# Kernel tuning notes

Measured on AMD Instinct MI355X. Metric: run time of the kernel, lower is better.

The kernel has to match this reference:

```python
import jax, jax.numpy as jnp
import numpy as np

N = 50000    # nodes
P = 4        # meta-paths
E = 800000   # edges per meta-path (avg degree 16)
IN = 256     # in_size
OUT = 128    # out_size


def _xavier(key, shape, gain=1.0):
    fan_in, fan_out = shape[-2], shape[-1]
    lim = gain * np.sqrt(6.0 / (fan_in + fan_out))
    return jax.random.uniform(key, shape, jnp.float32, -lim, lim)


def setup_inputs() -> dict:
    key = jax.random.key(0)
    ks = jax.random.split(key, 8)
    x = jax.random.normal(ks[0], (N, IN), jnp.float32)
    src = jax.random.randint(ks[1], (P, E), 0, N)
    dst = jax.random.randint(ks[2], (P, E), 0, N)
    # per-meta-path GraphConv weight/bias (dgl default: xavier weight, zero bias)
    W = _xavier(ks[3], (P, IN, OUT))
    b_conv = jnp.zeros((P, OUT), jnp.float32)
    # semantic attention vectors, xavier with gain=1.414 on shape (1, OUT)
    att_lim = 1.414 * np.sqrt(6.0 / (1 + OUT))
    att = jax.random.uniform(ks[4], (P, OUT), jnp.float32, -att_lim, att_lim)
    fc_w = _xavier(ks[5], (OUT, OUT))
    fc_b = jnp.zeros((OUT,), jnp.float32)
    h_bias = jnp.zeros((OUT,), jnp.float32)
    return {"x": x, "W": W, "b_conv": b_conv, "att": att,
            "fc_w": fc_w, "fc_b": fc_b, "h_bias": h_bias,
            "src": src, "dst": dst}


def _graphconv(x, src, dst, W, b):
    # dgl GraphConv, norm='both', allow_zero_in_degree=True (degrees clamped to 1)
    ones_e = jnp.ones(src.shape[0], x.dtype)
    deg_out = jnp.maximum(jax.ops.segment_sum(ones_e, src, num_segments=N), 1.0)
    deg_in = jnp.maximum(jax.ops.segment_sum(ones_e, dst, num_segments=N), 1.0)
    # weight applied before aggregation (in_size > out_size path) -- same math
    xw = (x * jax.lax.rsqrt(deg_out)[:, None]) @ W          # [N, OUT]
    agg = jax.ops.segment_sum(xw[src], dst, num_segments=N)  # [N, OUT]
    return agg * jax.lax.rsqrt(deg_in)[:, None] + b


def reference(x, W, b_conv, att, fc_w, fc_b, h_bias, src, dst):
    # one GraphConv per meta-path (P is a small fixed structural set)
    hs = [_graphconv(x, src[i], dst[i], W[i], b_conv[i]) for i in range(P)]
    # semantic attention: sp_i = tanh(fc(h_i)).mean(0); beta_i = att_i . sp_i
    sp = jnp.stack([jnp.tanh(h @ fc_w.T + fc_b).mean(axis=0) for h in hs])  # [P, OUT]
    beta = jax.nn.softmax(jnp.sum(att * sp, axis=-1))  # [P]
    h = hs[0] * beta[0]
    for i in range(1, P):
        h = h + hs[i] * beta[i]
    # epilogue: bias (self_loop=False, activation=None, dropout eval = identity)
    return h + h_bias
```

## Files before the change

### kernel.cpp

```cpp
#include <hip/hip_runtime.h>
#include <math.h>

#define N_NODES 50000
#define P_PATHS 4
#define E_EDGES 800000
#define IN_F 256
#define OUT_F 128
#define NPB 128
#define NBUCK 391
#define NCHUNK 200
#define CHUNK_E (E_EDGES / NCHUNK)
#define GBLK 391
#define DSL 20
#define QTR 4
#define Q_N 12500
#define Q_W 6250
#define BKP 72
#define FP 136
#define RSB 196

typedef unsigned short ushort_t;
typedef unsigned int uint_t;
typedef float f32x4 __attribute__((ext_vector_type(4)));
typedef short s16x8 __attribute__((ext_vector_type(8)));

__device__ __forceinline__ ushort_t f2bf(float f) {
    uint_t u = __float_as_uint(f);
    return (ushort_t)((u + 0x7FFFu + ((u >> 16) & 1u)) >> 16);
}
__device__ __forceinline__ float bf2f(ushort_t h) {
    return __uint_as_float(((uint_t)h) << 16);
}
__device__ __forceinline__ uint4 pack8(const float4 f0, const float4 f1) {
    uint4 w;
    w.x = (uint_t)f2bf(f0.x) | ((uint_t)f2bf(f0.y) << 16);
    w.y = (uint_t)f2bf(f0.z) | ((uint_t)f2bf(f0.w) << 16);
    w.z = (uint_t)f2bf(f1.x) | ((uint_t)f2bf(f1.y) << 16);
    w.w = (uint_t)f2bf(f1.z) | ((uint_t)f2bf(f1.w) << 16);
    return w;
}
__device__ __forceinline__ float fast_tanh(float v) {
    v = fminf(fmaxf(v, -20.f), 20.f);
    float ex = __expf(2.f * v);
    return (ex - 1.f) / (ex + 1.f);
}
__device__ __forceinline__ void acc4(float4& a, uint2 w) {
    a.x += bf2f((ushort_t)w.x);
    a.y += bf2f((ushort_t)(w.x >> 16));
    a.z += bf2f((ushort_t)w.y);
    a.w += bf2f((ushort_t)(w.y >> 16));
}

__global__ void prep_kernel(const float* __restrict__ W, const float* __restrict__ fcw,
                            ushort_t* __restrict__ Wt, ushort_t* __restrict__ fcwb)
{
    int idx = blockIdx.x * blockDim.x + threadIdx.x;
    if (idx < P_PATHS * IN_F * OUT_F) {
        int p = idx >> 15;
        int r = idx & 32767;
        int k = r >> 7;
        int n = r & 127;
        Wt[((size_t)p << 15) + (size_t)n * IN_F + k] = f2bf(W[idx]);
    }
    if (idx < OUT_F * OUT_F) fcwb[idx] = f2bf(fcw[idx]);
}

__global__ __launch_bounds__(256) void deghist_kernel(const int* __restrict__ src,
                                                      const int* __restrict__ dst,
                                                      uint_t* __restrict__ dhist,
                                                      uint_t* __restrict__ bcounts)
{
    __shared__ uint_t cnt[Q_W];
    int sl = blockIdx.x, q = blockIdx.y, p = blockIdx.z;
    int t = threadIdx.x;
    if (q == QTR) {
        for (int i = t; i < NBUCK; i += 256) cnt[i] = 0;
        __syncthreads();
        const int4* d4 = (const int4*)(dst + (size_t)p * E_EDGES + (size_t)sl * (E_EDGES / DSL));
        for (int i = t; i < E_EDGES / DSL / 4; i += 256) {
            int4 v = d4[i];
            atomicAdd(&cnt[v.x >> 7], 1u);
            atomicAdd(&cnt[v.y >> 7], 1u);
            atomicAdd(&cnt[v.z >> 7], 1u);
            atomicAdd(&cnt[v.w >> 7], 1u);
        }
        __syncthreads();
        for (int i = t; i < NBUCK; i += 256)
            if (cnt[i]) atomicAdd(&bcounts[p * NBUCK + i], cnt[i]);
        return;
    }
    int nbase = q * Q_N;
    for (int i = t; i < Q_W; i += 256) cnt[i] = 0;
    __syncthreads();
    const int4* s4 = (const int4*)(src + (size_t)p * E_EDGES + (size_t)sl * (E_EDGES / DSL));
    for (int i = t; i < E_EDGES / DSL / 4; i += 256) {
        int4 v = s4[i];
        uint_t r;
        r = (uint_t)(v.x - nbase); if (r < Q_N) atomicAdd(&cnt[r >> 1], 1u << ((r & 1) * 16));
        r = (uint_t)(v.y - nbase); if (r < Q_N) atomicAdd(&cnt[r >> 1], 1u << ((r & 1) * 16));
        r = (uint_t)(v.z - nbase); if (r < Q_N) atomicAdd(&cnt[r >> 1], 1u << ((r & 1) * 16));
        r = (uint_t)(v.w - nbase); if (r < Q_N) atomicAdd(&cnt[r >> 1], 1u << ((r & 1) * 16));
    }
    __syncthreads();
    uint_t* outp = dhist + (((size_t)p * QTR + q) * DSL + sl) * Q_W;
    for (int i = t; i < Q_W; i += 256) outp[i] = cnt[i];
}

__global__ __launch_bounds__(1024) void rsout_bscan_kernel(const uint_t* __restrict__ dhist,
                                                           float* __restrict__ rsout,
                                                           const uint_t* __restrict__ bcounts,
                                                           int* __restrict__ bstart,
                                                           int* __restrict__ bcursor)
{
    int t = threadIdx.x;
    if (blockIdx.x == RSB) {
        __shared__ int a[2048], b[2048];
        for (int i = t; i < 2048; i += 1024)
            a[i] = (i < P_PATHS * NBUCK) ? (int)bcounts[i] : 0;
        __syncthreads();
        int* pin = a; int* pout = b;
        for (int off = 1; off < 2048; off <<= 1) {
            for (int i = t; i < 2048; i += 1024)
                pout[i] = pin[i] + (i >= off ? pin[i - off] : 0);
            __syncthreads();
            int* tmp = pin; pin = pout; pout = tmp;
        }
        for (int i = t; i < P_PATHS * NBUCK; i += 1024) {
            int st = pin[i] - (int)bcounts[i];
            bstart[i] = st;
            bcursor[i] = st;
        }
        if (t == 0) bstart[P_PATHS * NBUCK] = pin[P_PATHS * NBUCK - 1];
        return;
    }
    int idx = blockIdx.x * 1024 + t;
    if (idx >= P_PATHS * QTR * Q_W) return;
    int ph = idx / Q_W;
    int w  = idx % Q_W;
    const uint_t* base = dhist + (size_t)ph * DSL * Q_W + w;
    uint_t s = 0;
#pragma unroll
    for (int sl = 0; sl < DSL; ++sl) s += base[(size_t)sl * Q_W];
    int p = ph >> 2, q = ph & 3;
    int node = q * Q_N + 2 * w;
    uint_t c0 = s & 0xFFFFu, c1 = s >> 16;
    rsout[(size_t)p * N_NODES + node]     = rsqrtf((float)(c0 ? c0 : 1u));
    rsout[(size_t)p * N_NODES + node + 1] = rsqrtf((float)(c1 ? c1 : 1u));
}

__global__ __launch_bounds__(256) void bscatter_kernel(const int* __restrict__ src,
                                                       const int* __restrict__ dst,
                                                       int* __restrict__ bcursor,
                                                       uint_t* __restrict__ ebuf)
{
    __shared__ uint_t bh[NBUCK];
    __shared__ uint_t lbase[NBUCK];
    int p = blockIdx.y;
    int t = threadIdx.x;
    int sub = p * E_EDGES;
    int* bcursor_p = bcursor + p * NBUCK;
    uint_t* ebuf_p = ebuf + (size_t)p * E_EDGES;
    for (int i = t; i < NBUCK; i += 256) bh[i] = 0;
    __syncthreads();
    size_t ebase = (size_t)p * E_EDGES + (size_t)blockIdx.x * CHUNK_E;
    const int4* d4 = (const int4*)(dst + ebase);
    const int4* s4 = (const int4*)(src + ebase);
    for (int i = t; i < CHUNK_E / 4; i += 256) {
        int4 v = d4[i];
        atomicAdd(&bh[v.x >> 7], 1u);
        atomicAdd(&bh[v.y >> 7], 1u);
        atomicAdd(&bh[v.z >> 7], 1u);
        atomicAdd(&bh[v.w >> 7], 1u);
    }
    __syncthreads();
    for (int i = t; i < NBUCK; i += 256) {
        uint_t c = bh[i];
        lbase[i] = c ? (uint_t)(atomicAdd(&bcursor_p[i], (int)c) - sub) : 0u;
        bh[i] = 0;
    }
    __syncthreads();
    for (int i = t; i < CHUNK_E / 4; i += 256) {
        int4 d = d4[i];
        int4 s = s4[i];
        { int bk = d.x >> 7; uint_t pos = lbase[bk] + atomicAdd(&bh[bk], 1u); ebuf_p[pos] = (uint_t)s.x | ((uint_t)(d.x & 127) << 16); }
        { int bk = d.y >> 7; uint_t pos = lbase[bk] + atomicAdd(&bh[bk], 1u); ebuf_p[pos] = (uint_t)s.y | ((uint_t)(d.y & 127) << 16); }
        { int bk = d.z >> 7; uint_t pos = lbase[bk] + atomicAdd(&bh[bk], 1u); ebuf_p[pos] = (uint_t)s.z | ((uint_t)(d.z & 127) << 16); }
        { int bk = d.w >> 7; uint_t pos = lbase[bk] + atomicAdd(&bh[bk], 1u); ebuf_p[pos] = (uint_t)s.w | ((uint_t)(d.w & 127) << 16); }
    }
}

__global__ __launch_bounds__(256) void blocal_kernel(const uint_t* __restrict__ ebuf,
                                                     const int* __restrict__ bstart,
                                                     ushort_t* __restrict__ eidx2,
                                                     int* __restrict__ rsn)
{
    __shared__ uint_t hist[NPB];
    __shared__ uint_t cur[NPB];
    __shared__ uint_t sa[NPB], sb[NPB];
    int bkt = blockIdx.x;
    int p = blockIdx.y;
    int t = threadIdx.x;
    int sub = p * E_EDGES;
    const uint_t* ebuf_p = ebuf + (size_t)p * E_EDGES;
    ushort_t* eidx2_p = eidx2 + (size_t)p * E_EDGES;
    int* rsn_p = rsn + (size_t)p * (N_NODES + 1);
    if (t < NPB) hist[t] = 0;
    __syncthreads();
    int r0 = bstart[p * NBUCK + bkt] - sub;
    int r1 = bstart[p * NBUCK + bkt + 1] - sub;
    for (int e = r0 + t; e < r1; e += 256)
        atomicAdd(&hist[ebuf_p[e] >> 16], 1u);
    __syncthreads();
    if (t < NPB) sa[t] = hist[t];
    __syncthreads();
    uint_t* pin = sa; uint_t* pout = sb;
    for (int off = 1; off < NPB; off <<= 1) {
        if (t < NPB) pout[t] = pin[t] + (t >= off ? pin[t - off] : 0u);
        __syncthreads();
        uint_t* tmp = pin; pin = pout; pout = tmp;
    }
    if (t < NPB) {
        uint_t ex = pin[t] - hist[t];
        int node = bkt * NPB + t;
        if (node < N_NODES) rsn_p[node] = r0 + (int)ex;
        cur[t] = ex;
    }
    if (bkt == NBUCK - 1 && t == 0) rsn_p[N_NODES] = r1;
    __syncthreads();
    for (int e = r0 + t; e < r1; e += 256) {
        uint_t pk = ebuf_p[e];
        int dl = (int)(pk >> 16);
        uint_t pos = atomicAdd(&cur[dl], 1u);
        eidx2_p[r0 + pos] = (ushort_t)(pk & 0xFFFFu);
    }
}

__global__ __launch_bounds__(256) void gemm_xall_kernel(const float* __restrict__ x,
                                                        const ushort_t* __restrict__ Wt,
                                                        const float* __restrict__ rsout,
                                                        ushort_t* __restrict__ xwb)
{
    __shared__ ushort_t As[128 * BKP];
    __shared__ ushort_t Bs[128 * BKP];
    int m0 = blockIdx.x * 128;
    int t = threadIdx.x;
    int wid = t >> 6, lane = t & 63;
    int wr = wid >> 1, wc = wid & 1;
    int srow = t >> 1, h32 = (t & 1) * 32;
    int gr = m0 + srow;
    for (int pp = 0; pp < 2; ++pp) {
        int p = blockIdx.y * 2 + pp;
        const ushort_t* Wp = Wt + ((size_t)p << 15);
        f32x4 acc[4][4] = {};
        for (int kt = 0; kt < 4; ++kt) {
            __syncthreads();
            {
                const float* ap = x + (size_t)gr * IN_F + kt * 64 + h32;
#pragma unroll
                for (int c = 0; c < 4; ++c) {
                    float4 f0 = make_float4(0.f, 0.f, 0.f, 0.f), f1 = f0;
                    if (gr < N_NODES) {
                        f0 = *(const float4*)(ap + c * 8);
                        f1 = *(const float4*)(ap + c * 8 + 4);
                    }
                    *(uint4*)&As[srow * BKP + h32 + c * 8] = pack8(f0, f1);
                }
            }
            {
                const ushort_t* bp = Wp + (size_t)srow * IN_F + kt * 64 + h32;
#pragma unroll
                for (int c = 0; c < 4; ++c)
                    *(uint4*)&Bs[srow * BKP + h32 + c * 8] = *(const uint4*)(bp + c * 8);
            }
            __syncthreads();
#pragma unroll
            for (int k0 = 0; k0 < 64; k0 += 32) {
                s16x8 aF[4], bF[4];
                int kk = k0 + (lane >> 4) * 8;
#pragma unroll
                for (int m = 0; m < 4; ++m)
                    aF[m] = *(const s16x8*)&As[(wr * 64 + m * 16 + (lane & 15)) * BKP + kk];
#pragma unroll
                for (int n = 0; n < 4; ++n)
                    bF[n] = *(const s16x8*)&Bs[(wc * 64 + n * 16 + (lane & 15)) * BKP + kk];
#pragma unroll
                for (int m = 0; m < 4; ++m)
#pragma unroll
                    for (int n = 0; n < 4; ++n)
                        acc[m][n] = __builtin_amdgcn_mfma_f32_16x16x32_bf16(aF[m], bF[n], acc[m][n], 0, 0, 0);
            }
        }
        ushort_t* xp = xwb + (size_t)p * N_NODES * OUT_F;
        const float* rp = rsout + (size_t)p * N_NODES;
#pragma unroll
        for (int m = 0; m < 4; ++m) {
#pragma unroll
            for (int i = 0; i < 4; ++i) {
                int row = m0 + wr * 64 + m * 16 + (lane >> 4) * 4 + i;
                if (row < N_NODES) {
                    float rs = rp[row];
#pragma unroll
                    for (int n = 0; n < 4; ++n) {
                        int col = wc * 64 + n * 16 + (lane & 15);
                        xp[(size_t)row * OUT_F + col] = f2bf(acc[m][n][i] * rs);
                    }
                }
            }
        }
    }
}

__global__ __launch_bounds__(256) void gather_kernel(const ushort_t* __restrict__ xwb,
                                                     const ushort_t* __restrict__ eidx2,
                                                     const int* __restrict__ rsn,
                                                     const float* __restrict__ bconv,
                                                     uint2* __restrict__ hb)
{
    int hw = threadIdx.x >> 5;
    int lane = threadIdx.x & 31;
    int p = blockIdx.y;
    int n0 = (blockIdx.x * 8 + hw) * 2;
    const int* rsn_p = rsn + (size_t)p * (N_NODES + 1);
    const ushort_t* eidx2_p = eidx2 + (size_t)p * E_EDGES;
    int bA = rsn_p[n0], mid = rsn_p[n0 + 1], eB = rsn_p[n0 + 2];
    const uint2* base = (const uint2*)xwb + (size_t)p * N_NODES * 32 + lane;
    float4 aA = make_float4(0.f, 0.f, 0.f, 0.f);
    float4 aB = make_float4(0.f, 0.f, 0.f, 0.f);
    int iA = bA, iB = mid;
    while (iA + 4 <= mid && iB + 4 <= eB) {
        int sA0 = eidx2_p[iA], sA1 = eidx2_p[iA + 1], sA2 = eidx2_p[iA + 2], sA3 = eidx2_p[iA + 3];
        int sB0 = eidx2_p[iB], sB1 = eidx2_p[iB + 1], sB2 = eidx2_p[iB + 2], sB3 = eidx2_p[iB + 3];
        uint2 wA0 = base[(size_t)sA0 * 32];
        uint2 wA1 = base[(size_t)sA1 * 32];
        uint2 wA2 = base[(size_t)sA2 * 32];
        uint2 wA3 = base[(size_t)sA3 * 32];
        uint2 wB0 = base[(size_t)sB0 * 32];
        uint2 wB1 = base[(size_t)sB1 * 32];
        uint2 wB2 = base[(size_t)sB2 * 32];
        uint2 wB3 = base[(size_t)sB3 * 32];
        acc4(aA, wA0); acc4(aA, wA1); acc4(aA, wA2); acc4(aA, wA3);
        acc4(aB, wB0); acc4(aB, wB1); acc4(aB, wB2); acc4(aB, wB3);
        iA += 4; iB += 4;
    }
    for (; iA + 4 <= mid; iA += 4) {
        int s0 = eidx2_p[iA], s1 = eidx2_p[iA + 1], s2 = eidx2_p[iA + 2], s3 = eidx2_p[iA + 3];
        uint2 w0 = base[(size_t)s0 * 32];
        uint2 w1 = base[(size_t)s1 * 32];
        uint2 w2 = base[(size_t)s2 * 32];
        uint2 w3 = base[(size_t)s3 * 32];
        acc4(aA, w0); acc4(aA, w1); acc4(aA, w2); acc4(aA, w3);
    }
    for (; iA < mid; ++iA) {
        uint2 w = base[(size_t)eidx2_p[iA] * 32];
        acc4(aA, w);
    }
    for (; iB + 4 <= eB; iB += 4) {
        int s0 = eidx2_p[iB], s1 = eidx2_p[iB + 1], s2 = eidx2_p[iB + 2], s3 = eidx2_p[iB + 3];
        uint2 w0 = base[(size_t)s0 * 32];
        uint2 w1 = base[(size_t)s1 * 32];
        uint2 w2 = base[(size_t)s2 * 32];
        uint2 w3 = base[(size_t)s3 * 32];
        acc4(aB, w0); acc4(aB, w1); acc4(aB, w2); acc4(aB, w3);
    }
    for (; iB < eB; ++iB) {
        uint2 w = base[(size_t)eidx2_p[iB] * 32];
        acc4(aB, w);
    }
    int dA = mid - bA, dB = eB - mid;
    float scA = rsqrtf((float)(dA > 0 ? dA : 1));
    float scB = rsqrtf((float)(dB > 0 ? dB : 1));
    float4 bc = *(const float4*)(bconv + (size_t)p * OUT_F + lane * 4);
    uint2 oA, oB;
    oA.x = (uint_t)f2bf(fmaf(aA.x, scA, bc.x)) | ((uint_t)f2bf(fmaf(aA.y, scA, bc.y)) << 16);
    oA.y = (uint_t)f2bf(fmaf(aA.z, scA, bc.z)) | ((uint_t)f2bf(fmaf(aA.w, scA, bc.w)) << 16);
    oB.x = (uint_t)f2bf(fmaf(aB.x, scB, bc.x)) | ((uint_t)f2bf(fmaf(aB.y, scB, bc.y)) << 16);
    oB.y = (uint_t)f2bf(fmaf(aB.z, scB, bc.z)) | ((uint_t)f2bf(fmaf(aB.w, scB, bc.w)) << 16);
    hb[((size_t)p * N_NODES + n0) * 32 + lane]     = oA;
    hb[((size_t)p * N_NODES + n0 + 1) * 32 + lane] = oB;
}

__global__ __launch_bounds__(256) void fc_mfma_kernel(const ushort_t* __restrict__ hb,
                                                      const ushort_t* __restrict__ fcwb,
                                                      const float* __restrict__ fcb,
                                                      float* __restrict__ partial)
{
    __shared__ ushort_t As[128 * FP];
    __shared__ ushort_t Bs[128 * FP];
    __shared__ float red[2][128];
    int m0 = blockIdx.x * 128;
    int t = threadIdx.x;
    int wid = t >> 6, lane = t & 63;
    int wr = wid >> 1, wc = wid & 1;
    int srow = t >> 1, half = (t & 1) * 16;
    int gr = m0 + srow;
    {
#pragma unroll
        for (int c = 0; c < 4; ++c) {
            int kb = c * 32 + half;
            const ushort_t* bp = fcwb + (size_t)srow * OUT_F + kb;
            *(uint4*)&Bs[srow * FP + kb]     = *(const uint4*)(bp);
            *(uint4*)&Bs[srow * FP + kb + 8] = *(const uint4*)(bp + 8);
        }
    }
    for (int p = 0; p < P_PATHS; ++p) {
        __syncthreads();
        const ushort_t* hp = hb + (size_t)p * N_NODES * OUT_F;
#pragma unroll
        for (int c = 0; c < 4; ++c) {
            int kb = c * 32 + half;
            uint4 w0 = make_uint4(0, 0, 0, 0), w1 = w0;
            if (gr < N_NODES) {
                const ushort_t* ap = hp + (size_t)gr * OUT_F + kb;
                w0 = *(const uint4*)(ap);
                w1 = *(const uint4*)(ap + 8);
            }
            *(uint4*)&As[srow * FP + kb]     = w0;
            *(uint4*)&As[srow * FP + kb + 8] = w1;
        }
        __syncthreads();
        f32x4 acc[4][4] = {};
#pragma unroll
        for (int k0 = 0; k0 < OUT_F; k0 += 32) {
            s16x8 aF[4], bF[4];
            int kk = k0 + (lane >> 4) * 8;
#pragma unroll
            for (int m = 0; m < 4; ++m)
                aF[m] = *(const s16x8*)&As[(wr * 64 + m * 16 + (lane & 15)) * FP + kk];
#pragma unroll
            for (int n = 0; n < 4; ++n)
                bF[n] = *(const s16x8*)&Bs[(wc * 64 + n * 16 + (lane & 15)) * FP + kk];
#pragma unroll
            for (int m = 0; m < 4; ++m)
#pragma unroll
                for (int n = 0; n < 4; ++n)
                    acc[m][n] = __builtin_amdgcn_mfma_f32_16x16x32_bf16(aF[m], bF[n], acc[m][n], 0, 0, 0);
        }
#pragma unroll
        for (int n = 0; n < 4; ++n) {
            int col = wc * 64 + n * 16 + (lane & 15);
            float fb = fcb[col];
            float s = 0.f;
#pragma unroll
            for (int m = 0; m < 4; ++m)
#pragma unroll
                for (int i = 0; i < 4; ++i) {
                    int row = m0 + wr * 64 + m * 16 + (lane >> 4) * 4 + i;
                    if (row < N_NODES) s += fast_tanh(acc[m][n][i] + fb);
                }
            s += __shfl_xor(s, 16);
            s += __shfl_xor(s, 32);
            if (lane < 16) red[wr][col] = s;
        }
        __syncthreads();
        if (t < 128)
            partial[((size_t)p * GBLK + blockIdx.x) * OUT_F + t] = red[0][t] + red[1][t];
    }
}

__global__ __launch_bounds__(512) void beta_reduce_kernel(const float* __restrict__ partial,
                                                          const float* __restrict__ att,
                                                          float* __restrict__ beta)
{
    int t = threadIdx.x;
    int p = t >> 7, c = t & 127;
    float s = 0.f;
    for (int i = 0; i < GBLK; ++i)
        s += partial[((size_t)p * GBLK + i) * OUT_F + c];
    float v = att[p * OUT_F + c] * (s * (1.0f / N_NODES));
    __shared__ float red[512];
    red[t] = v;
    __syncthreads();
    for (int off = 64; off >= 1; off >>= 1) {
        if (c < off) red[t] += red[t + off];
        __syncthreads();
    }
    if (t == 0) {
        float w[P_PATHS], mx = -1e30f;
        for (int q = 0; q < P_PATHS; ++q) { w[q] = red[q * 128]; mx = fmaxf(mx, w[q]); }
        float sum = 0.f;
        for (int q = 0; q < P_PATHS; ++q) { w[q] = expf(w[q] - mx); sum += w[q]; }
        for (int q = 0; q < P_PATHS; ++q) beta[q] = w[q] / sum;
    }
}

__global__ void combine_kernel(const uint_t* __restrict__ hb, const float* __restrict__ hbias,
                               const float* __restrict__ beta, float* __restrict__ out)
{
    int idx = blockIdx.x * blockDim.x + threadIdx.x;
    if (idx >= N_NODES * 64) return;
    int n = idx >> 6;
    int w = idx & 63;
    float2 hbv = *(const float2*)(hbias + 2 * w);
    float r0 = hbv.x, r1 = hbv.y;
#pragma unroll
    for (int p = 0; p < P_PATHS; ++p) {
        float bp = beta[p];
        uint_t v = hb[((size_t)p * N_NODES + n) * 64 + w];
        r0 = fmaf(bp, bf2f((ushort_t)v), r0);
        r1 = fmaf(bp, bf2f((ushort_t)(v >> 16)), r1);
    }
    *(float2*)(out + (size_t)n * OUT_F + 2 * w) = make_float2(r0, r1);
}

extern "C" void kernel_launch(void* const* d_in, const int* in_sizes, int n_in,
                              void* d_out, int out_size, void* d_ws, size_t ws_size,
                              hipStream_t stream)
{
    const float* x      = (const float*)d_in[0];
    const float* W      = (const float*)d_in[1];
    const float* b_conv = (const float*)d_in[2];
    const float* att    = (const float*)d_in[3];
    const float* fc_w   = (const float*)d_in[4];
    const float* fc_b   = (const float*)d_in[5];
    const float* h_bias = (const float*)d_in[6];
    const int*   src    = (const int*)d_in[7];
    const int*   dst    = (const int*)d_in[8];
    float* out = (float*)d_out;
    float* ws  = (float*)d_ws;

    size_t off_rsout   = 0;
    size_t off_partial = off_rsout + (size_t)P_PATHS * N_NODES;
    size_t off_beta    = off_partial + (size_t)P_PATHS * GBLK * OUT_F;
    size_t off_i32     = (off_beta + 4 + 63) & ~(size_t)63;
    size_t i_bstart  = 0;
    size_t i_bcursor = 1600;
    size_t i_bcounts = 3200;
    size_t i_rsn     = 4800;
    size_t i_dhist   = 204864;
    size_t i_ebuf    = i_dhist + (size_t)P_PATHS * QTR * DSL * Q_W;
    size_t n_ints    = i_ebuf + (size_t)P_PATHS * E_EDGES;
    size_t off_u16   = off_i32 + ((n_ints + 63) & ~(size_t)63);
    size_t u_hb    = 0;
    size_t u_xwb   = u_hb + (size_t)P_PATHS * N_NODES * OUT_F;
    size_t u_eidx2 = u_xwb + (size_t)P_PATHS * N_NODES * OUT_F;
    size_t u_Wt    = u_eidx2 + (size_t)P_PATHS * E_EDGES;
    size_t u_fcwb  = u_Wt + (size_t)P_PATHS * IN_F * OUT_F;

    float* rsout   = ws + off_rsout;
    float* partial = ws + off_partial;
    float* beta    = ws + off_beta;
    int*   ibase   = (int*)(ws + off_i32);
    int*    bstart  = ibase + i_bstart;
    int*    bcursor = ibase + i_bcursor;
    uint_t* bcounts = (uint_t*)(ibase + i_bcounts);
    int*    rsn     = ibase + i_rsn;
    uint_t* dhist   = (uint_t*)(ibase + i_dhist);
    uint_t* ebuf    = (uint_t*)(ibase + i_ebuf);
    ushort_t* ubase = (ushort_t*)(ws + off_u16);
    ushort_t* hb    = ubase + u_hb;
    ushort_t* xwb   = ubase + u_xwb;
    ushort_t* eidx2 = ubase + u_eidx2;
    ushort_t* Wt    = ubase + u_Wt;
    ushort_t* fcwb  = ubase + u_fcwb;

    hipMemsetAsync(bcounts, 0, (size_t)P_PATHS * NBUCK * sizeof(uint_t), stream);

    prep_kernel<<<(P_PATHS * IN_F * OUT_F + 255) / 256, 256, 0, stream>>>(W, fc_w, Wt, fcwb);
    deghist_kernel<<<dim3(DSL, QTR + 1, P_PATHS), 256, 0, stream>>>(src, dst, dhist, bcounts);
    rsout_bscan_kernel<<<RSB + 1, 1024, 0, stream>>>(dhist, rsout, bcounts, bstart, bcursor);

    gemm_xall_kernel<<<dim3(GBLK, 2), 256, 0, stream>>>(x, Wt, rsout, xwb);
    bscatter_kernel<<<dim3(NCHUNK, P_PATHS), 256, 0, stream>>>(src, dst, bcursor, ebuf);
    blocal_kernel<<<dim3(NBUCK, P_PATHS), 256, 0, stream>>>(ebuf, bstart, eidx2, rsn);
    gather_kernel<<<dim3(N_NODES / 16, P_PATHS), 256, 0, stream>>>(
        xwb, eidx2, rsn, b_conv, (uint2*)hb);
    fc_mfma_kernel<<<GBLK, 256, 0, stream>>>(hb, fcwb, fc_b, partial);

    beta_reduce_kernel<<<1, 512, 0, stream>>>(partial, att, beta);
    combine_kernel<<<(N_NODES * 64 + 255) / 256, 256, 0, stream>>>(
        (const uint_t*)hb, h_bias, beta, out);
}
```

Measured before the change: 316.6 us.

## Fuse prep into deghist, merge gemm with bscatter, widen gather loads

```diff
diff --git a/kernel.cpp b/kernel.cpp
--- a/kernel.cpp
+++ b/kernel.cpp
@@ -44,35 +44,38 @@
     float ex = __expf(2.f * v);
     return (ex - 1.f) / (ex + 1.f);
 }
-__device__ __forceinline__ void acc4(float4& a, uint2 w) {
-    a.x += bf2f((ushort_t)w.x);
-    a.y += bf2f((ushort_t)(w.x >> 16));
-    a.z += bf2f((ushort_t)w.y);
-    a.w += bf2f((ushort_t)(w.y >> 16));
-}
-
-__global__ void prep_kernel(const float* __restrict__ W, const float* __restrict__ fcw,
-                            ushort_t* __restrict__ Wt, ushort_t* __restrict__ fcwb)
-{
-    int idx = blockIdx.x * blockDim.x + threadIdx.x;
-    if (idx < P_PATHS * IN_F * OUT_F) {
-        int p = idx >> 15;
-        int r = idx & 32767;
-        int k = r >> 7;
-        int n = r & 127;
-        Wt[((size_t)p << 15) + (size_t)n * IN_F + k] = f2bf(W[idx]);
-    }
-    if (idx < OUT_F * OUT_F) fcwb[idx] = f2bf(fcw[idx]);
+__device__ __forceinline__ void acc8(float4& a0, float4& a1, uint4 w) {
+    a0.x += bf2f((ushort_t)w.x);  a0.y += bf2f((ushort_t)(w.x >> 16));
+    a0.z += bf2f((ushort_t)w.y);  a0.w += bf2f((ushort_t)(w.y >> 16));
+    a1.x += bf2f((ushort_t)w.z);  a1.y += bf2f((ushort_t)(w.z >> 16));
+    a1.z += bf2f((ushort_t)w.w);  a1.w += bf2f((ushort_t)(w.w >> 16));
 }
 
 __global__ __launch_bounds__(256) void deghist_kernel(const int* __restrict__ src,
                                                       const int* __restrict__ dst,
                                                       uint_t* __restrict__ dhist,
-                                                      uint_t* __restrict__ bcounts)
+                                                      uint_t* __restrict__ bcounts,
+                                                      const float* __restrict__ W,
+                                                      const float* __restrict__ fcw,
+                                                      ushort_t* __restrict__ Wt,
+                                                      ushort_t* __restrict__ fcwb)
 {
     __shared__ uint_t cnt[Q_W];
     int sl = blockIdx.x, q = blockIdx.y, p = blockIdx.z;
     int t = threadIdx.x;
+    if (q == QTR + 1) {
+        int g = (p * DSL + sl) * 256 + t;
+        for (int idx = g; idx < P_PATHS * IN_F * OUT_F; idx += DSL * P_PATHS * 256) {
+            int pp = idx >> 15;
+            int r = idx & 32767;
+            int k = r >> 7;
+            int n = r & 127;
+            Wt[((size_t)pp << 15) + (size_t)n * IN_F + k] = f2bf(W[idx]);
+        }
+        for (int idx = g; idx < OUT_F * OUT_F; idx += DSL * P_PATHS * 256)
+            fcwb[idx] = f2bf(fcw[idx]);
+        return;
+    }
     if (q == QTR) {
         for (int i = t; i < NBUCK; i += 256) cnt[i] = 0;
         __syncthreads();
@@ -148,21 +151,100 @@
     rsout[(size_t)p * N_NODES + node + 1] = rsqrtf((float)(c1 ? c1 : 1u));
 }
 
-__global__ __launch_bounds__(256) void bscatter_kernel(const int* __restrict__ src,
-                                                       const int* __restrict__ dst,
-                                                       int* __restrict__ bcursor,
-                                                       uint_t* __restrict__ ebuf)
-{
-    __shared__ uint_t bh[NBUCK];
-    __shared__ uint_t lbase[NBUCK];
-    int p = blockIdx.y;
+__global__ __launch_bounds__(256) void mid_kernel(const float* __restrict__ x,
+                                                  const ushort_t* __restrict__ Wt,
+                                                  const float* __restrict__ rsout,
+                                                  ushort_t* __restrict__ xwb,
+                                                  const int* __restrict__ src,
+                                                  const int* __restrict__ dst,
+                                                  int* __restrict__ bcursor,
+                                                  uint_t* __restrict__ ebuf)
+{
+    __shared__ ushort_t smem[2 * 128 * BKP];
+    int bx = blockIdx.x;
     int t = threadIdx.x;
+    if (bx < 2 * GBLK) {
+        ushort_t* As = smem;
+        ushort_t* Bs = smem + 128 * BKP;
+        int m0 = (bx % GBLK) * 128;
+        int pair = bx / GBLK;
+        int wid = t >> 6, lane = t & 63;
+        int wr = wid >> 1, wc = wid & 1;
+        int srow = t >> 1, h32 = (t & 1) * 32;
+        int gr = m0 + srow;
+        for (int pp = 0; pp < 2; ++pp) {
+            int p = pair * 2 + pp;
+            const ushort_t* Wp = Wt + ((size_t)p << 15);
+            f32x4 acc[4][4] = {};
+            for (int kt = 0; kt < 4; ++kt) {
+                __syncthreads();
+                {
+                    const float* ap = x + (size_t)gr * IN_F + kt * 64 + h32;
+#pragma unroll
+                    for (int c = 0; c < 4; ++c) {
+                        float4 f0 = make_float4(0.f, 0.f, 0.f, 0.f), f1 = f0;
+                        if (gr < N_NODES) {
+                            f0 = *(const float4*)(ap + c * 8);
+                            f1 = *(const float4*)(ap + c * 8 + 4);
+                        }
+                        *(uint4*)&As[srow * BKP + h32 + c * 8] = pack8(f0, f1);
+                    }
+                }
+                {
+                    const ushort_t* bp = Wp + (size_t)srow * IN_F + kt * 64 + h32;
+#pragma unroll
+                    for (int c = 0; c < 4; ++c)
+                        *(uint4*)&Bs[srow * BKP + h32 + c * 8] = *(const uint4*)(bp + c * 8);
+                }
+                __syncthreads();
+#pragma unroll
+                for (int k0 = 0; k0 < 64; k0 += 32) {
+                    s16x8 aF[4], bF[4];
+                    int kk = k0 + (lane >> 4) * 8;
+#pragma unroll
+                    for (int m = 0; m < 4; ++m)
+                        aF[m] = *(const s16x8*)&As[(wr * 64 + m * 16 + (lane & 15)) * BKP + kk];
+#pragma unroll
+                    for (int n = 0; n < 4; ++n)
+                        bF[n] = *(const s16x8*)&Bs[(wc * 64 + n * 16 + (lane & 15)) * BKP + kk];
+#pragma unroll
+                    for (int m = 0; m < 4; ++m)
+#pragma unroll
+                        for (int n = 0; n < 4; ++n)
+                            acc[m][n] = __builtin_amdgcn_mfma_f32_16x16x32_bf16(aF[m], bF[n], acc[m][n], 0, 0, 0);
+                }
+            }
+            ushort_t* xp = xwb + (size_t)p * N_NODES * OUT_F;
+            const float* rp = rsout + (size_t)p * N_NODES;
+#pragma unroll
+            for (int m = 0; m < 4; ++m) {
+#pragma unroll
+                for (int i = 0; i < 4; ++i) {
+                    int row = m0 + wr * 64 + m * 16 + (lane >> 4) * 4 + i;
+                    if (row < N_NODES) {
+                        float rs = rp[row];
+#pragma unroll
+                        for (int n = 0; n < 4; ++n) {
+                            int col = wc * 64 + n * 16 + (lane & 15);
+                            xp[(size_t)row * OUT_F + col] = f2bf(acc[m][n][i] * rs);
+                        }
+                    }
+                }
+            }
+        }
+        return;
+    }
+    int idx = bx - 2 * GBLK;
+    int p = idx / NCHUNK;
+    int ck = idx % NCHUNK;
+    uint_t* bh    = (uint_t*)smem;
+    uint_t* lbase = bh + NBUCK;
     int sub = p * E_EDGES;
     int* bcursor_p = bcursor + p * NBUCK;
     uint_t* ebuf_p = ebuf + (size_t)p * E_EDGES;
     for (int i = t; i < NBUCK; i += 256) bh[i] = 0;
     __syncthreads();
-    size_t ebase = (size_t)p * E_EDGES + (size_t)blockIdx.x * CHUNK_E;
+    size_t ebase = (size_t)p * E_EDGES + (size_t)ck * CHUNK_E;
     const int4* d4 = (const int4*)(dst + ebase);
     const int4* s4 = (const int4*)(src + ebase);
     for (int i = t; i < CHUNK_E / 4; i += 256) {
@@ -235,148 +317,62 @@
     }
 }
 
-__global__ __launch_bounds__(256) void gemm_xall_kernel(const float* __restrict__ x,
-                                                        const ushort_t* __restrict__ Wt,
-                                                        const float* __restrict__ rsout,
-                                                        ushort_t* __restrict__ xwb)
-{
-    __shared__ ushort_t As[128 * BKP];
-    __shared__ ushort_t Bs[128 * BKP];
-    int m0 = blockIdx.x * 128;
-    int t = threadIdx.x;
-    int wid = t >> 6, lane = t & 63;
-    int wr = wid >> 1, wc = wid & 1;
-    int srow = t >> 1, h32 = (t & 1) * 32;
-    int gr = m0 + srow;
-    for (int pp = 0; pp < 2; ++pp) {
-        int p = blockIdx.y * 2 + pp;
-        const ushort_t* Wp = Wt + ((size_t)p << 15);
-        f32x4 acc[4][4] = {};
-        for (int kt = 0; kt < 4; ++kt) {
-            __syncthreads();
-            {
-                const float* ap = x + (size_t)gr * IN_F + kt * 64 + h32;
-#pragma unroll
-                for (int c = 0; c < 4; ++c) {
-                    float4 f0 = make_float4(0.f, 0.f, 0.f, 0.f), f1 = f0;
-                    if (gr < N_NODES) {
-                        f0 = *(const float4*)(ap + c * 8);
-                        f1 = *(const float4*)(ap + c * 8 + 4);
-                    }
-                    *(uint4*)&As[srow * BKP + h32 + c * 8] = pack8(f0, f1);
-                }
-            }
-            {
-                const ushort_t* bp = Wp + (size_t)srow * IN_F + kt * 64 + h32;
-#pragma unroll
-                for (int c = 0; c < 4; ++c)
-                    *(uint4*)&Bs[srow * BKP + h32 + c * 8] = *(const uint4*)(bp + c * 8);
-            }
-            __syncthreads();
-#pragma unroll
-            for (int k0 = 0; k0 < 64; k0 += 32) {
-                s16x8 aF[4], bF[4];
-                int kk = k0 + (lane >> 4) * 8;
-#pragma unroll
-                for (int m = 0; m < 4; ++m)
-                    aF[m] = *(const s16x8*)&As[(wr * 64 + m * 16 + (lane & 15)) * BKP + kk];
-#pragma unroll
-                for (int n = 0; n < 4; ++n)
-                    bF[n] = *(const s16x8*)&Bs[(wc * 64 + n * 16 + (lane & 15)) * BKP + kk];
-#pragma unroll
-                for (int m = 0; m < 4; ++m)
-#pragma unroll
-                    for (int n = 0; n < 4; ++n)
-                        acc[m][n] = __builtin_amdgcn_mfma_f32_16x16x32_bf16(aF[m], bF[n], acc[m][n], 0, 0, 0);
-            }
-        }
-        ushort_t* xp = xwb + (size_t)p * N_NODES * OUT_F;
-        const float* rp = rsout + (size_t)p * N_NODES;
-#pragma unroll
-        for (int m = 0; m < 4; ++m) {
-#pragma unroll
-            for (int i = 0; i < 4; ++i) {
-                int row = m0 + wr * 64 + m * 16 + (lane >> 4) * 4 + i;
-                if (row < N_NODES) {
-                    float rs = rp[row];
-#pragma unroll
-                    for (int n = 0; n < 4; ++n) {
-                        int col = wc * 64 + n * 16 + (lane & 15);
-                        xp[(size_t)row * OUT_F + col] = f2bf(acc[m][n][i] * rs);
-                    }
-                }
-            }
-        }
-    }
-}
-
 __global__ __launch_bounds__(256) void gather_kernel(const ushort_t* __restrict__ xwb,
                                                      const ushort_t* __restrict__ eidx2,
                                                      const int* __restrict__ rsn,
                                                      const float* __restrict__ bconv,
-                                                     uint2* __restrict__ hb)
+                                                     uint4* __restrict__ hb)
 {
     int hw = threadIdx.x >> 5;
     int lane = threadIdx.x & 31;
+    int sub = lane >> 4;
+    int c16 = lane & 15;
     int p = blockIdx.y;
-    int n0 = (blockIdx.x * 8 + hw) * 2;
+    int n = blockIdx.x * 8 + hw;
     const int* rsn_p = rsn + (size_t)p * (N_NODES + 1);
-    const ushort_t* eidx2_p = eidx2 + (size_t)p * E_EDGES;
-    int bA = rsn_p[n0], mid = rsn_p[n0 + 1], eB = rsn_p[n0 + 2];
-    const uint2* base = (const uint2*)xwb + (size_t)p * N_NODES * 32 + lane;
-    float4 aA = make_float4(0.f, 0.f, 0.f, 0.f);
-    float4 aB = make_float4(0.f, 0.f, 0.f, 0.f);
-    int iA = bA, iB = mid;
-    while (iA + 4 <= mid && iB + 4 <= eB) {
-        int sA0 = eidx2_p[iA], sA1 = eidx2_p[iA + 1], sA2 = eidx2_p[iA + 2], sA3 = eidx2_p[iA + 3];
-        int sB0 = eidx2_p[iB], sB1 = eidx2_p[iB + 1], sB2 = eidx2_p[iB + 2], sB3 = eidx2_p[iB + 3];
-        uint2 wA0 = base[(size_t)sA0 * 32];
-        uint2 wA1 = base[(size_t)sA1 * 32];
-        uint2 wA2 = base[(size_t)sA2 * 32];
-        uint2 wA3 = base[(size_t)sA3 * 32];
-        uint2 wB0 = base[(size_t)sB0 * 32];
-        uint2 wB1 = base[(size_t)sB1 * 32];
-        uint2 wB2 = base[(size_t)sB2 * 32];
-        uint2 wB3 = base[(size_t)sB3 * 32];
-        acc4(aA, wA0); acc4(aA, wA1); acc4(aA, wA2); acc4(aA, wA3);
-        acc4(aB, wB0); acc4(aB, wB1); acc4(aB, wB2); acc4(aB, wB3);
-        iA += 4; iB += 4;
-    }
-    for (; iA + 4 <= mid; iA += 4) {
-        int s0 = eidx2_p[iA], s1 = eidx2_p[iA + 1], s2 = eidx2_p[iA + 2], s3 = eidx2_p[iA + 3];
-        uint2 w0 = base[(size_t)s0 * 32];
-        uint2 w1 = base[(size_t)s1 * 32];
-        uint2 w2 = base[(size_t)s2 * 32];
-        uint2 w3 = base[(size_t)s3 * 32];
-        acc4(aA, w0); acc4(aA, w1); acc4(aA, w2); acc4(aA, w3);
-    }
-    for (; iA < mid; ++iA) {
-        uint2 w = base[(size_t)eidx2_p[iA] * 32];
-        acc4(aA, w);
-    }
-    for (; iB + 4 <= eB; iB += 4) {
-        int s0 = eidx2_p[iB], s1 = eidx2_p[iB + 1], s2 = eidx2_p[iB + 2], s3 = eidx2_p[iB + 3];
-        uint2 w0 = base[(size_t)s0 * 32];
-        uint2 w1 = base[(size_t)s1 * 32];
-        uint2 w2 = base[(size_t)s2 * 32];
-        uint2 w3 = base[(size_t)s3 * 32];
-        acc4(aB, w0); acc4(aB, w1); acc4(aB, w2); acc4(aB, w3);
-    }
-    for (; iB < eB; ++iB) {
-        uint2 w = base[(size_t)eidx2_p[iB] * 32];
-        acc4(aB, w);
-    }
-    int dA = mid - bA, dB = eB - mid;
-    float scA = rsqrtf((float)(dA > 0 ? dA : 1));
-    float scB = rsqrtf((float)(dB > 0 ? dB : 1));
-    float4 bc = *(const float4*)(bconv + (size_t)p * OUT_F + lane * 4);
-    uint2 oA, oB;
-    oA.x = (uint_t)f2bf(fmaf(aA.x, scA, bc.x)) | ((uint_t)f2bf(fmaf(aA.y, scA, bc.y)) << 16);
-    oA.y = (uint_t)f2bf(fmaf(aA.z, scA, bc.z)) | ((uint_t)f2bf(fmaf(aA.w, scA, bc.w)) << 16);
-    oB.x = (uint_t)f2bf(fmaf(aB.x, scB, bc.x)) | ((uint_t)f2bf(fmaf(aB.y, scB, bc.y)) << 16);
-    oB.y = (uint_t)f2bf(fmaf(aB.z, scB, bc.z)) | ((uint_t)f2bf(fmaf(aB.w, scB, bc.w)) << 16);
-    hb[((size_t)p * N_NODES + n0) * 32 + lane]     = oA;
-    hb[((size_t)p * N_NODES + n0 + 1) * 32 + lane] = oB;
+    const ushort_t* ei = eidx2 + (size_t)p * E_EDGES;
+    int b = rsn_p[n], e = rsn_p[n + 1];
+    const uint4* base = (const uint4*)xwb + (size_t)p * N_NODES * 16 + c16;
+    float4 a0 = make_float4(0.f, 0.f, 0.f, 0.f);
+    float4 a1 = make_float4(0.f, 0.f, 0.f, 0.f);
+    int i = b;
+    for (; i + 8 <= e; i += 8) {
+        int s0 = ei[i + sub];
+        int s1 = ei[i + 2 + sub];
+        int s2 = ei[i + 4 + sub];
+        int s3 = ei[i + 6 + sub];
+        uint4 w0 = base[(size_t)s0 * 16];
+        uint4 w1 = base[(size_t)s1 * 16];
+        uint4 w2 = base[(size_t)s2 * 16];
+        uint4 w3 = base[(size_t)s3 * 16];
+        acc8(a0, a1, w0); acc8(a0, a1, w1); acc8(a0, a1, w2); acc8(a0, a1, w3);
+    }
+    for (; i + 2 <= e; i += 2) {
+        int s = ei[i + sub];
+        uint4 w = base[(size_t)s * 16];
+        acc8(a0, a1, w);
+    }
+    if (i < e && sub == 0) {
+        int s = ei[i];
+        uint4 w = base[(size_t)s * 16];
+        acc8(a0, a1, w);
+    }
+    a0.x += __shfl_xor(a0.x, 16); a0.y += __shfl_xor(a0.y, 16);
+    a0.z += __shfl_xor(a0.z, 16); a0.w += __shfl_xor(a0.w, 16);
+    a1.x += __shfl_xor(a1.x, 16); a1.y += __shfl_xor(a1.y, 16);
+    a1.z += __shfl_xor(a1.z, 16); a1.w += __shfl_xor(a1.w, 16);
+    if (sub == 0) {
+        int d = e - b;
+        float sc = rsqrtf((float)(d > 0 ? d : 1));
+        float4 bc0 = *(const float4*)(bconv + (size_t)p * OUT_F + c16 * 8);
+        float4 bc1 = *(const float4*)(bconv + (size_t)p * OUT_F + c16 * 8 + 4);
+        uint4 o;
+        o.x = (uint_t)f2bf(fmaf(a0.x, sc, bc0.x)) | ((uint_t)f2bf(fmaf(a0.y, sc, bc0.y)) << 16);
+        o.y = (uint_t)f2bf(fmaf(a0.z, sc, bc0.z)) | ((uint_t)f2bf(fmaf(a0.w, sc, bc0.w)) << 16);
+        o.z = (uint_t)f2bf(fmaf(a1.x, sc, bc1.x)) | ((uint_t)f2bf(fmaf(a1.y, sc, bc1.y)) << 16);
+        o.w = (uint_t)f2bf(fmaf(a1.z, sc, bc1.z)) | ((uint_t)f2bf(fmaf(a1.w, sc, bc1.w)) << 16);
+        hb[((size_t)p * N_NODES + n) * 16 + c16] = o;
+    }
 }
 
 __global__ __launch_bounds__(256) void fc_mfma_kernel(const ushort_t* __restrict__ hb,
@@ -457,26 +453,31 @@
     }
 }
 
-__global__ __launch_bounds__(512) void beta_reduce_kernel(const float* __restrict__ partial,
-                                                          const float* __restrict__ att,
-                                                          float* __restrict__ beta)
+__global__ __launch_bounds__(1024) void beta_reduce_kernel(const float* __restrict__ partial,
+                                                           const float* __restrict__ att,
+                                                           float* __restrict__ beta)
 {
     int t = threadIdx.x;
-    int p = t >> 7, c = t & 127;
+    int p = t >> 8;
+    int r = t & 255;
+    int c = r & 127;
+    int hf = r >> 7;
     float s = 0.f;
-    for (int i = 0; i < GBLK; ++i)
+    for (int i = hf; i < GBLK; i += 2)
         s += partial[((size_t)p * GBLK + i) * OUT_F + c];
-    float v = att[p * OUT_F + c] * (s * (1.0f / N_NODES));
-    __shared__ float red[512];
-    red[t] = v;
+    __shared__ float red[1024];
+    red[t] = s;
+    __syncthreads();
+    if (hf == 0)
+        red[t] = (red[t] + red[t + 128]) * att[p * OUT_F + c] * (1.0f / N_NODES);
     __syncthreads();
     for (int off = 64; off >= 1; off >>= 1) {
-        if (c < off) red[t] += red[t + off];
+        if (hf == 0 && c < off) red[t] += red[t + off];
         __syncthreads();
     }
     if (t == 0) {
         float w[P_PATHS], mx = -1e30f;
-        for (int q = 0; q < P_PATHS; ++q) { w[q] = red[q * 128]; mx = fmaxf(mx, w[q]); }
+        for (int q = 0; q < P_PATHS; ++q) { w[q] = red[q * 256]; mx = fmaxf(mx, w[q]); }
         float sum = 0.f;
         for (int q = 0; q < P_PATHS; ++q) { w[q] = expf(w[q] - mx); sum += w[q]; }
         for (int q = 0; q < P_PATHS; ++q) beta[q] = w[q] / sum;
@@ -555,18 +556,18 @@
 
     hipMemsetAsync(bcounts, 0, (size_t)P_PATHS * NBUCK * sizeof(uint_t), stream);
 
-    prep_kernel<<<(P_PATHS * IN_F * OUT_F + 255) / 256, 256, 0, stream>>>(W, fc_w, Wt, fcwb);
-    deghist_kernel<<<dim3(DSL, QTR + 1, P_PATHS), 256, 0, stream>>>(src, dst, dhist, bcounts);
+    deghist_kernel<<<dim3(DSL, QTR + 2, P_PATHS), 256, 0, stream>>>(
+        src, dst, dhist, bcounts, W, fc_w, Wt, fcwb);
     rsout_bscan_kernel<<<RSB + 1, 1024, 0, stream>>>(dhist, rsout, bcounts, bstart, bcursor);
 
-    gemm_xall_kernel<<<dim3(GBLK, 2), 256, 0, stream>>>(x, Wt, rsout, xwb);
-    bscatter_kernel<<<dim3(NCHUNK, P_PATHS), 256, 0, stream>>>(src, dst, bcursor, ebuf);
+    mid_kernel<<<2 * GBLK + NCHUNK * P_PATHS, 256, 0, stream>>>(
+        x, Wt, rsout, xwb, src, dst, bcursor, ebuf);
     blocal_kernel<<<dim3(NBUCK, P_PATHS), 256, 0, stream>>>(ebuf, bstart, eidx2, rsn);
-    gather_kernel<<<dim3(N_NODES / 16, P_PATHS), 256, 0, stream>>>(
-        xwb, eidx2, rsn, b_conv, (uint2*)hb);
+    gather_kernel<<<dim3(N_NODES / 8, P_PATHS), 256, 0, stream>>>(
+        xwb, eidx2, rsn, b_conv, (uint4*)hb);
     fc_mfma_kernel<<<GBLK, 256, 0, stream>>>(hb, fcwb, fc_b, partial);
 
-    beta_reduce_kernel<<<1, 512, 0, stream>>>(partial, att, beta);
+    beta_reduce_kernel<<<1, 1024, 0, stream>>>(partial, att, beta);
     combine_kernel<<<(N_NODES * 64 + 255) / 256, 256, 0, stream>>>(
         (const uint_t*)hb, h_bias, beta, out);
 }
```

New measurement: 331.2 us. 1.05x slower.
